# Performance work log

Measured on AMD Instinct MI355X. Metric: run time of the kernel, lower is better.

## Reference

```python
import jax, jax.numpy as jnp
import numpy as np

N_TABLES = 26
VOCAB = 100000
M_SPA = 64
B = 8192
N_DENSE = 13
N_FEAT = N_TABLES + 1  # 27 features entering interaction
LI, LJ = np.tril_indices(N_FEAT, k=-1)  # strictly-lower pairs, matches torch li/lj order


def setup_inputs() -> dict:
    key = jax.random.key(0)
    ks = jax.random.split(key, 16)
    dense_x = jax.random.normal(ks[0], (B, N_DENSE), dtype=jnp.float32)
    lS_i = jax.random.randint(ks[1], (N_TABLES, B), 0, VOCAB, dtype=jnp.int64)
    # one index per bag -> offsets are arange(B) for every table
    lS_o = jnp.tile(jnp.arange(B, dtype=jnp.int64)[None, :], (N_TABLES, 1))
    # embedding tables, uniform(-sqrt(1/n), sqrt(1/n)) as in create_emb
    s = np.sqrt(1.0 / VOCAB)
    Wemb = jax.random.uniform(ks[2], (N_TABLES, VOCAB, M_SPA), dtype=jnp.float32, minval=-s, maxval=s)

    def mk_lin(k, n, m):
        k1, k2 = jax.random.split(k)
        W = jax.random.normal(k1, (m, n), dtype=jnp.float32) * np.sqrt(2.0 / (m + n))
        b = jax.random.normal(k2, (m,), dtype=jnp.float32) * np.sqrt(1.0 / m)
        return W, b

    bW0, bb0 = mk_lin(ks[3], 13, 512)
    bW1, bb1 = mk_lin(ks[4], 512, 256)
    bW2, bb2 = mk_lin(ks[5], 256, 64)
    tW0, tb0 = mk_lin(ks[6], 415, 512)
    tW1, tb1 = mk_lin(ks[7], 512, 256)
    tW2, tb2 = mk_lin(ks[8], 256, 1)
    return dict(dense_x=dense_x, lS_i=lS_i, lS_o=lS_o, Wemb=Wemb,
                bW0=bW0, bb0=bb0, bW1=bW1, bb1=bb1, bW2=bW2, bb2=bb2,
                tW0=tW0, tb0=tb0, tW1=tW1, tb1=tb1, tW2=tW2, tb2=tb2)


def reference(dense_x, lS_i, lS_o, Wemb,
              bW0, bb0, bW1, bb1, bW2, bb2,
              tW0, tb0, tW1, tb1, tW2, tb2):
    # bottom MLP (all ReLU, sigmoid_bot=-1)
    x = jax.nn.relu(dense_x @ bW0.T + bb0)
    x = jax.nn.relu(x @ bW1.T + bb1)
    x = jax.nn.relu(x @ bW2.T + bb2)  # [B, 64]
    # multi-table EmbeddingBag(sum) with one index per bag == plain gather
    ly = jax.vmap(lambda W, idx: W[idx])(Wemb, lS_i)  # [26, B, 64]
    # dot interaction
    T = jnp.concatenate([x[:, None, :], jnp.transpose(ly, (1, 0, 2))], axis=1)  # [B, 27, 64]
    Z = jnp.einsum('bnd,bmd->bnm', T, T)  # [B, 27, 27]
    Zflat = Z[:, LI, LJ]  # [B, 351]
    R = jnp.concatenate([x, Zflat], axis=1)  # [B, 415]
    # top MLP: ReLU, ReLU, Sigmoid (sigmoid_top=2)
    z = jax.nn.relu(R @ tW0.T + tb0)
    z = jax.nn.relu(z @ tW1.T + tb1)
    p = jax.nn.sigmoid(z @ tW2.T + tb2)  # [B, 1]
    # loss_threshold = 0.0 -> no clamp
    return p
```

## Files before the change

### kernel.cpp

```cpp
#include <hip/hip_runtime.h>
#include <hip/hip_bf16.h>


typedef _Float16 f16x8 __attribute__((ext_vector_type(8)));
typedef float f32x4 __attribute__((ext_vector_type(4)));

__device__ __forceinline__ f16x8 cvt8(float4 a, float4 b) {
  f16x8 f;
  f[0] = (_Float16)a.x; f[1] = (_Float16)a.y;
  f[2] = (_Float16)a.z; f[3] = (_Float16)a.w;
  f[4] = (_Float16)b.x; f[5] = (_Float16)b.y;
  f[6] = (_Float16)b.z; f[7] = (_Float16)b.w;
  return f;
}

__device__ __forceinline__ void frag_store(
    _Float16* __restrict__ dst, const float* __restrict__ src,
    int fl, int Ksrc, int NKK)
{
  int lane = fl & 63, q = fl >> 6;
  int kk = q % NKK, j = q / NKK;
  int c = j * 16 + (lane & 15);
  int kb = kk * 32 + (lane >> 4) * 8;
  const float* s = src + (size_t)c * Ksrc + kb;
  f16x8 o;
#pragma unroll
  for (int e = 0; e < 8; ++e)
    o[e] = (_Float16)((kb + e < Ksrc) ? s[e] : 0.0f);
  *(f16x8*)&dst[(size_t)fl * 8] = o;
}

__global__ __launch_bounds__(256) void prep_kernel(
    const float* __restrict__ bW0, const float* __restrict__ bW1,
    const float* __restrict__ bW2, const float* __restrict__ tW0,
    const float* __restrict__ tW1,
    _Float16* __restrict__ w0, _Float16* __restrict__ w1,
    _Float16* __restrict__ w2, _Float16* __restrict__ t0,
    _Float16* __restrict__ t1)
{
  int f = blockIdx.x * 256 + threadIdx.x;
  if (f < 2048)  { frag_store(w0, bW0, f, 13, 1);  return; }
  f -= 2048;
  if (f < 16384) { frag_store(w1, bW1, f, 512, 16); return; }
  f -= 16384;
  if (f < 2048)  { frag_store(w2, bW2, f, 256, 8);  return; }
  f -= 2048;
  if (f < 28672) { frag_store(t0, tW0, f, 415, 14); return; }
  f -= 28672;
  if (f < 16384) { frag_store(t1, tW1, f, 512, 16); return; }
}

__global__ __launch_bounds__(1024, 1) void fused_kernel(
    const float* __restrict__ dense, const int* __restrict__ lSi,
    const float* __restrict__ Wemb,
    const _Float16* __restrict__ w0, const float* __restrict__ bb0,
    const _Float16* __restrict__ w1, const float* __restrict__ bb1,
    const _Float16* __restrict__ w2, const float* __restrict__ bb2,
    const _Float16* __restrict__ t0w, const float* __restrict__ tb0,
    const _Float16* __restrict__ t1w, const float* __restrict__ tb1,
    const float* __restrict__ tW2, const float* __restrict__ tb2,
    float* __restrict__ out)
{
  __shared__ __align__(16) char regA[32768];
  __shared__ __align__(16) char regB[28672];
  _Float16* x1s = (_Float16*)regA;
  _Float16* x3s = (_Float16*)regA;
  _Float16* z1s = (_Float16*)regA;
  float*    dns = (float*)regB;
  _Float16* x2s = (_Float16*)regB;
  _Float16* Rs  = (_Float16*)regB;
  float*    psm = (float*)regB;

  const int t = threadIdx.x;
  const int lane = t & 63, wv = t >> 6;
  const int rc = lane & 15, g = lane >> 4;
  const int ko = g * 8;
  const int sw = (rc & 7) << 3;
  const int b0 = blockIdx.x * 32;

  if (t < 416) {
    int r = t / 13, c = t - r * 13;
    dns[r * 16 + c] = dense[(size_t)b0 * 13 + t];
  } else if (t < 512) {
    int q = t - 416;
    int r = q / 3, c = 13 + (q - r * 3);
    dns[r * 16 + c] = 0.0f;
  }
  __syncthreads();

  {
    f16x8 af[2];
#pragma unroll
    for (int rt = 0; rt < 2; ++rt) {
      f16x8 a = {};
      if (g < 2) {
        const float* s = &dns[(rt * 16 + rc) * 16 + ko];
        a = cvt8(*(const float4*)s, *(const float4*)(s + 4));
      }
      af[rt] = a;
    }
    f32x4 acc[2][2] = {};
#pragma unroll
    for (int j = 0; j < 2; ++j) {
      const int jb = wv * 2 + j;
      f16x8 wf = *(const f16x8*)&w0[(size_t)(jb * 64 + lane) * 8];
#pragma unroll
      for (int rt = 0; rt < 2; ++rt)
        acc[rt][j] = __builtin_amdgcn_mfma_f32_16x16x32_f16(af[rt], wf, acc[rt][j], 0, 0, 0);
    }
#pragma unroll
    for (int j = 0; j < 2; ++j) {
      const int col = wv * 32 + j * 16 + rc;
      const float bs = bb0[col];
#pragma unroll
      for (int rt = 0; rt < 2; ++rt)
#pragma unroll
        for (int r = 0; r < 4; ++r) {
          int row = rt * 16 + g * 4 + r;
          float v = fmaxf(acc[rt][j][r] + bs, 0.0f);
          x1s[row * 512 + (col ^ ((row & 7) << 3))] = (_Float16)v;
        }
    }
  }
  __syncthreads();

  {
    f32x4 acc[2] = {};
#pragma unroll
    for (int kk = 0; kk < 16; ++kk) {
      f16x8 af[2];
#pragma unroll
      for (int rt = 0; rt < 2; ++rt)
        af[rt] = *(const f16x8*)&x1s[(rt * 16 + rc) * 512 + ((kk * 32 + ko) ^ sw)];
      f16x8 wf = *(const f16x8*)&w1[(size_t)((wv * 16 + kk) * 64 + lane) * 8];
#pragma unroll
      for (int rt = 0; rt < 2; ++rt)
        acc[rt] = __builtin_amdgcn_mfma_f32_16x16x32_f16(af[rt], wf, acc[rt], 0, 0, 0);
    }
    const int col = wv * 16 + rc;
    const float bs = bb1[col];
#pragma unroll
    for (int rt = 0; rt < 2; ++rt)
#pragma unroll
      for (int r = 0; r < 4; ++r) {
        int row = rt * 16 + g * 4 + r;
        float v = fmaxf(acc[rt][r] + bs, 0.0f);
        x2s[row * 256 + (col ^ ((row & 7) << 3))] = (_Float16)v;
      }
  }
  __syncthreads();

  if (wv < 8) {
    const int rt = wv & 1;
    const int cb = (wv >> 1) * 16;
    f32x4 acc = {};
#pragma unroll
    for (int kk = 0; kk < 8; ++kk) {
      f16x8 af = *(const f16x8*)&x2s[(rt * 16 + rc) * 256 + ((kk * 32 + ko) ^ sw)];
      f16x8 wf = *(const f16x8*)&w2[(size_t)(((cb >> 4) * 8 + kk) * 64 + lane) * 8];
      acc = __builtin_amdgcn_mfma_f32_16x16x32_f16(af, wf, acc, 0, 0, 0);
    }
    const int col = cb + rc;
    const float bs = bb2[col];
#pragma unroll
    for (int r = 0; r < 4; ++r) {
      int row = rt * 16 + g * 4 + r;
      float v = fmaxf(acc[r] + bs, 0.0f);
      x3s[row * 64 + col] = (_Float16)v;
    }
  }
  __syncthreads();

  {
    int e_idx[2][2];
#pragma unroll
    for (int i = 0; i < 2; ++i) {
      const int b = b0 + wv * 2 + i;
#pragma unroll
      for (int rt = 0; rt < 2; ++rt) {
        const int gr = rt * 16 + rc;
        e_idx[i][rt] = (gr >= 1 && gr <= 26) ? lSi[(size_t)(gr - 1) * 8192 + b] : 0;
      }
    }
#pragma unroll
    for (int i = 0; i < 2; ++i) {
      const int bl = wv * 2 + i;
      const int swr = (bl & 7) << 3;
      f16x8 frag[2][2];
#pragma unroll
      for (int rt = 0; rt < 2; ++rt) {
        const int gr = rt * 16 + rc;
        if (gr == 0) {
          frag[rt][0] = *(const f16x8*)&x3s[bl * 64 + ko];
          frag[rt][1] = *(const f16x8*)&x3s[bl * 64 + 32 + ko];
        } else if (gr <= 26) {
          const float* src = Wemb + ((size_t)(gr - 1) * 100000 + (size_t)e_idx[i][rt]) * 64;
#pragma unroll
          for (int kh = 0; kh < 2; ++kh) {
            const float* s = src + kh * 32 + ko;
            frag[rt][kh] = cvt8(*(const float4*)s, *(const float4*)(s + 4));
          }
        } else {
          f16x8 z = {};
          frag[rt][0] = z; frag[rt][1] = z;
        }
      }
      f32x4 z00 = {}, z10 = {}, z11 = {};
#pragma unroll
      for (int kh = 0; kh < 2; ++kh) {
        z00 = __builtin_amdgcn_mfma_f32_16x16x32_f16(frag[0][kh], frag[0][kh], z00, 0, 0, 0);
        z10 = __builtin_amdgcn_mfma_f32_16x16x32_f16(frag[1][kh], frag[0][kh], z10, 0, 0, 0);
        z11 = __builtin_amdgcn_mfma_f32_16x16x32_f16(frag[1][kh], frag[1][kh], z11, 0, 0, 0);
      }
      Rs[bl * 448 + (lane ^ swr)] = x3s[bl * 64 + lane];
      if (lane < 33) Rs[bl * 448 + ((415 + lane) ^ swr)] = (_Float16)0.0f;
      const int col = lane & 15;
      const int rr0 = (lane >> 4) * 4;
#pragma unroll
      for (int r = 0; r < 4; ++r) {
        const int i0 = rr0 + r;
        if (i0 > col) {
          int p = 64 + i0 * (i0 - 1) / 2 + col;
          Rs[bl * 448 + (p ^ swr)] = (_Float16)z00[r];
        }
        const int i1 = 16 + rr0 + r;
        if (i1 < 27) {
          int p = 64 + i1 * (i1 - 1) / 2 + col;
          Rs[bl * 448 + (p ^ swr)] = (_Float16)z10[r];
          const int j1 = 16 + col;
          if (i1 > j1) {
            int q = 64 + i1 * (i1 - 1) / 2 + j1;
            Rs[bl * 448 + (q ^ swr)] = (_Float16)z11[r];
          }
        }
      }
    }
  }
  __syncthreads();

  {
    f32x4 acc[2][2] = {};
#pragma unroll
    for (int kk = 0; kk < 14; ++kk) {
      f16x8 af[2];
#pragma unroll
      for (int rt = 0; rt < 2; ++rt)
        af[rt] = *(const f16x8*)&Rs[(rt * 16 + rc) * 448 + ((kk * 32 + ko) ^ sw)];
#pragma unroll
      for (int j = 0; j < 2; ++j) {
        const int jb = wv * 2 + j;
        f16x8 wf = *(const f16x8*)&t0w[(size_t)((jb * 14 + kk) * 64 + lane) * 8];
#pragma unroll
        for (int rt = 0; rt < 2; ++rt)
          acc[rt][j] = __builtin_amdgcn_mfma_f32_16x16x32_f16(af[rt], wf, acc[rt][j], 0, 0, 0);
      }
    }
#pragma unroll
    for (int j = 0; j < 2; ++j) {
      const int col = wv * 32 + j * 16 + rc;
      const float bs = tb0[col];
#pragma unroll
      for (int rt = 0; rt < 2; ++rt)
#pragma unroll
        for (int r = 0; r < 4; ++r) {
          int row = rt * 16 + g * 4 + r;
          float v = fmaxf(acc[rt][j][r] + bs, 0.0f);
          z1s[row * 512 + (col ^ ((row & 7) << 3))] = (_Float16)v;
        }
    }
  }
  __syncthreads();

  {
    f32x4 acc[2] = {};
#pragma unroll
    for (int kk = 0; kk < 16; ++kk) {
      f16x8 af[2];
#pragma unroll
      for (int rt = 0; rt < 2; ++rt)
        af[rt] = *(const f16x8*)&z1s[(rt * 16 + rc) * 512 + ((kk * 32 + ko) ^ sw)];
      f16x8 wf = *(const f16x8*)&t1w[(size_t)((wv * 16 + kk) * 64 + lane) * 8];
#pragma unroll
      for (int rt = 0; rt < 2; ++rt)
        acc[rt] = __builtin_amdgcn_mfma_f32_16x16x32_f16(af[rt], wf, acc[rt], 0, 0, 0);
    }
    const int col = wv * 16 + rc;
    const float bz = tb1[col];
    const float wz = tW2[col];
    float pd[2][4];
#pragma unroll
    for (int rt = 0; rt < 2; ++rt)
#pragma unroll
      for (int r = 0; r < 4; ++r)
        pd[rt][r] = fmaxf(acc[rt][r] + bz, 0.0f) * wz;
    __syncthreads();
#pragma unroll
    for (int rt = 0; rt < 2; ++rt)
#pragma unroll
      for (int r = 0; r < 4; ++r) {
        float v = pd[rt][r];
        v += __shfl_xor(v, 1, 64);
        v += __shfl_xor(v, 2, 64);
        v += __shfl_xor(v, 4, 64);
        v += __shfl_xor(v, 8, 64);
        if (rc == 0) psm[wv * 32 + rt * 16 + g * 4 + r] = v;
      }
  }
  __syncthreads();
  if (t < 32) {
    float s = tb2[0];
#pragma unroll
    for (int w = 0; w < 16; ++w) s += psm[w * 32 + t];
    out[b0 + t] = 1.0f / (1.0f + expf(-s));
  }
}

extern "C" void kernel_launch(void* const* d_in, const int* in_sizes, int n_in,
                              void* d_out, int out_size, void* d_ws, size_t ws_size,
                              hipStream_t stream)
{
  (void)in_sizes; (void)n_in; (void)out_size; (void)ws_size;
  const float* dense = (const float*)d_in[0];
  const int*   lSi   = (const int*)d_in[1];
  const float* Wemb  = (const float*)d_in[3];
  const float* bW0 = (const float*)d_in[4];  const float* bb0 = (const float*)d_in[5];
  const float* bW1 = (const float*)d_in[6];  const float* bb1 = (const float*)d_in[7];
  const float* bW2 = (const float*)d_in[8];  const float* bb2 = (const float*)d_in[9];
  const float* tW0 = (const float*)d_in[10]; const float* tb0 = (const float*)d_in[11];
  const float* tW1 = (const float*)d_in[12]; const float* tb1 = (const float*)d_in[13];
  const float* tW2 = (const float*)d_in[14]; const float* tb2 = (const float*)d_in[15];
  float* out = (float*)d_out;

  char* ws = (char*)d_ws;
  size_t off = 0;
  auto alloc = [&](size_t bytes) -> void* {
    void* p = ws + off;
    off += (bytes + 255) & ~(size_t)255;
    return p;
  };
  _Float16* w0 = (_Float16*)alloc((size_t)16384 * 2);
  _Float16* w1 = (_Float16*)alloc((size_t)131072 * 2);
  _Float16* w2 = (_Float16*)alloc((size_t)16384 * 2);
  _Float16* t0 = (_Float16*)alloc((size_t)229376 * 2);
  _Float16* t1 = (_Float16*)alloc((size_t)131072 * 2);

  prep_kernel<<<256, 256, 0, stream>>>(bW0, bW1, bW2, tW0, tW1,
                                       w0, w1, w2, t0, t1);
  fused_kernel<<<256, 1024, 0, stream>>>(dense, lSi, Wemb,
                                         w0, bb0, w1, bb1, w2, bb2,
                                         t0, tb0, t1, tb1, tW2, tb2, out);
}
```

Before: 36.66 us.

## Warp-specialize: prefetch half the embedding rows into LDS during bottom MLP

The bottom MLP now runs on only 8 of the 16 waves, each computing more output tiles. The other 8 waves issue asynchronous global-to-LDS loads (global_load_lds) for the first 12 tables' embedding rows while the MLP runs, and match its barriers with raw s_barrier calls. The interaction stage then reads those rows from swizzled LDS instead of global memory, so gather latency overlaps with MLP compute. In exchange it adds about 96KB of LDS and halves the MLP parallelism, and the barrier counts in the two branches must stay in lockstep.

Measured after the change: 36.70 us. Within noise of the previous version (+0.1%).

```diff
diff --git a/kernel.cpp b/kernel.cpp
--- a/kernel.cpp
+++ b/kernel.cpp
@@ -63,6 +63,7 @@
 {
   __shared__ __align__(16) char regA[32768];
   __shared__ __align__(16) char regB[28672];
+  __shared__ __align__(16) float embf[12 * 32 * 64];
   _Float16* x1s = (_Float16*)regA;
   _Float16* x3s = (_Float16*)regA;
   _Float16* z1s = (_Float16*)regA;
@@ -78,98 +79,142 @@
   const int sw = (rc & 7) << 3;
   const int b0 = blockIdx.x * 32;
 
-  if (t < 416) {
-    int r = t / 13, c = t - r * 13;
-    dns[r * 16 + c] = dense[(size_t)b0 * 13 + t];
-  } else if (t < 512) {
-    int q = t - 416;
-    int r = q / 3, c = 13 + (q - r * 3);
-    dns[r * 16 + c] = 0.0f;
-  }
-  __syncthreads();
-
-  {
-    f16x8 af[2];
-#pragma unroll
-    for (int rt = 0; rt < 2; ++rt) {
-      f16x8 a = {};
-      if (g < 2) {
-        const float* s = &dns[(rt * 16 + rc) * 16 + ko];
-        a = cvt8(*(const float4*)s, *(const float4*)(s + 4));
-      }
-      af[rt] = a;
-    }
-    f32x4 acc[2][2] = {};
-#pragma unroll
-    for (int j = 0; j < 2; ++j) {
-      const int jb = wv * 2 + j;
-      f16x8 wf = *(const f16x8*)&w0[(size_t)(jb * 64 + lane) * 8];
-#pragma unroll
-      for (int rt = 0; rt < 2; ++rt)
-        acc[rt][j] = __builtin_amdgcn_mfma_f32_16x16x32_f16(af[rt], wf, acc[rt][j], 0, 0, 0);
-    }
-#pragma unroll
-    for (int j = 0; j < 2; ++j) {
-      const int col = wv * 32 + j * 16 + rc;
-      const float bs = bb0[col];
+  if (wv < 8) {
+    if (t < 416) {
+      int r = t / 13, c = t - r * 13;
+      dns[r * 16 + c] = dense[(size_t)b0 * 13 + t];
+    } else if (t < 512) {
+      int q = t - 416;
+      int r = q / 3, c = 13 + (q - r * 3);
+      dns[r * 16 + c] = 0.0f;
+    }
+    __syncthreads();
+
+    {
+      f16x8 af[2];
+#pragma unroll
+      for (int rt = 0; rt < 2; ++rt) {
+        f16x8 a = {};
+        if (g < 2) {
+          const float* s = &dns[(rt * 16 + rc) * 16 + ko];
+          a = cvt8(*(const float4*)s, *(const float4*)(s + 4));
+        }
+        af[rt] = a;
+      }
+      f32x4 acc[2][4] = {};
+#pragma unroll
+      for (int j = 0; j < 4; ++j) {
+        const int jb = wv * 4 + j;
+        f16x8 wf = *(const f16x8*)&w0[(size_t)(jb * 64 + lane) * 8];
+#pragma unroll
+        for (int rt = 0; rt < 2; ++rt)
+          acc[rt][j] = __builtin_amdgcn_mfma_f32_16x16x32_f16(af[rt], wf, acc[rt][j], 0, 0, 0);
+      }
+#pragma unroll
+      for (int j = 0; j < 4; ++j) {
+        const int col = wv * 64 + j * 16 + rc;
+        const float bs = bb0[col];
+#pragma unroll
+        for (int rt = 0; rt < 2; ++rt)
+#pragma unroll
+          for (int r = 0; r < 4; ++r) {
+            int row = rt * 16 + g * 4 + r;
+            float v = fmaxf(acc[rt][j][r] + bs, 0.0f);
+            x1s[row * 512 + (col ^ ((row & 7) << 3))] = (_Float16)v;
+          }
+      }
+    }
+    __syncthreads();
+
+    {
+      f32x4 acc[2][2] = {};
+#pragma unroll
+      for (int kk = 0; kk < 16; ++kk) {
+        f16x8 af[2];
+#pragma unroll
+        for (int rt = 0; rt < 2; ++rt)
+          af[rt] = *(const f16x8*)&x1s[(rt * 16 + rc) * 512 + ((kk * 32 + ko) ^ sw)];
+#pragma unroll
+        for (int j = 0; j < 2; ++j) {
+          const int jb = wv * 2 + j;
+          f16x8 wf = *(const f16x8*)&w1[(size_t)((jb * 16 + kk) * 64 + lane) * 8];
+#pragma unroll
+          for (int rt = 0; rt < 2; ++rt)
+            acc[rt][j] = __builtin_amdgcn_mfma_f32_16x16x32_f16(af[rt], wf, acc[rt][j], 0, 0, 0);
+        }
+      }
+#pragma unroll
+      for (int j = 0; j < 2; ++j) {
+        const int col = wv * 32 + j * 16 + rc;
+        const float bs = bb1[col];
+#pragma unroll
+        for (int rt = 0; rt < 2; ++rt)
+#pragma unroll
+          for (int r = 0; r < 4; ++r) {
+            int row = rt * 16 + g * 4 + r;
+            float v = fmaxf(acc[rt][j][r] + bs, 0.0f);
+            x2s[row * 256 + (col ^ ((row & 7) << 3))] = (_Float16)v;
+          }
+      }
+    }
+    __syncthreads();
+
+    if (wv < 4) {
+      f32x4 acc[2] = {};
+#pragma unroll
+      for (int kk = 0; kk < 8; ++kk) {
+        f16x8 wf = *(const f16x8*)&w2[(size_t)((wv * 8 + kk) * 64 + lane) * 8];
+#pragma unroll
+        for (int rt = 0; rt < 2; ++rt) {
+          f16x8 af = *(const f16x8*)&x2s[(rt * 16 + rc) * 256 + ((kk * 32 + ko) ^ sw)];
+          acc[rt] = __builtin_amdgcn_mfma_f32_16x16x32_f16(af, wf, acc[rt], 0, 0, 0);
+        }
+      }
+      const int col = wv * 16 + rc;
+      const float bs = bb2[col];
 #pragma unroll
       for (int rt = 0; rt < 2; ++rt)
 #pragma unroll
         for (int r = 0; r < 4; ++r) {
           int row = rt * 16 + g * 4 + r;
-          float v = fmaxf(acc[rt][j][r] + bs, 0.0f);
-          x1s[row * 512 + (col ^ ((row & 7) << 3))] = (_Float16)v;
-        }
-    }
+          float v = fmaxf(acc[rt][r] + bs, 0.0f);
+          x3s[row * 64 + col] = (_Float16)v;
+        }
+    }
+    __syncthreads();
+  } else {
+    __builtin_amdgcn_s_barrier();
+    {
+      const int gw = wv - 8;
+      const int lhi = lane >> 4;
+      const int llo = lane & 15;
+      int idxv[12];
+#pragma unroll
+      for (int m = 0; m < 12; ++m) {
+        int q = gw * 12 + m;
+        int row = q * 4 + lhi;
+        int tb = row >> 5;
+        int bl = row & 31;
+        idxv[m] = lSi[(size_t)tb * 8192 + b0 + bl];
+      }
+#pragma unroll
+      for (int m = 0; m < 12; ++m) {
+        int q = gw * 12 + m;
+        int row = q * 4 + lhi;
+        int tb = row >> 5;
+        int cg = llo ^ (tb & 15);
+        const float* gp = Wemb + ((size_t)tb * 100000 + (size_t)idxv[m]) * 64 + cg * 4;
+        float* lp = &embf[q * 256];
+        __builtin_amdgcn_global_load_lds(
+            (const __attribute__((address_space(1))) void*)gp,
+            (__attribute__((address_space(3))) void*)lp, 16, 0, 0);
+      }
+    }
+    __builtin_amdgcn_s_barrier();
+    __builtin_amdgcn_s_barrier();
+    asm volatile("s_waitcnt vmcnt(0)" ::: "memory");
+    __builtin_amdgcn_s_barrier();
   }
-  __syncthreads();
-
-  {
-    f32x4 acc[2] = {};
-#pragma unroll
-    for (int kk = 0; kk < 16; ++kk) {
-      f16x8 af[2];
-#pragma unroll
-      for (int rt = 0; rt < 2; ++rt)
-        af[rt] = *(const f16x8*)&x1s[(rt * 16 + rc) * 512 + ((kk * 32 + ko) ^ sw)];
-      f16x8 wf = *(const f16x8*)&w1[(size_t)((wv * 16 + kk) * 64 + lane) * 8];
-#pragma unroll
-      for (int rt = 0; rt < 2; ++rt)
-        acc[rt] = __builtin_amdgcn_mfma_f32_16x16x32_f16(af[rt], wf, acc[rt], 0, 0, 0);
-    }
-    const int col = wv * 16 + rc;
-    const float bs = bb1[col];
-#pragma unroll
-    for (int rt = 0; rt < 2; ++rt)
-#pragma unroll
-      for (int r = 0; r < 4; ++r) {
-        int row = rt * 16 + g * 4 + r;
-        float v = fmaxf(acc[rt][r] + bs, 0.0f);
-        x2s[row * 256 + (col ^ ((row & 7) << 3))] = (_Float16)v;
-      }
-  }
-  __syncthreads();
-
-  if (wv < 8) {
-    const int rt = wv & 1;
-    const int cb = (wv >> 1) * 16;
-    f32x4 acc = {};
-#pragma unroll
-    for (int kk = 0; kk < 8; ++kk) {
-      f16x8 af = *(const f16x8*)&x2s[(rt * 16 + rc) * 256 + ((kk * 32 + ko) ^ sw)];
-      f16x8 wf = *(const f16x8*)&w2[(size_t)(((cb >> 4) * 8 + kk) * 64 + lane) * 8];
-      acc = __builtin_amdgcn_mfma_f32_16x16x32_f16(af, wf, acc, 0, 0, 0);
-    }
-    const int col = cb + rc;
-    const float bs = bb2[col];
-#pragma unroll
-    for (int r = 0; r < 4; ++r) {
-      int row = rt * 16 + g * 4 + r;
-      float v = fmaxf(acc[r] + bs, 0.0f);
-      x3s[row * 64 + col] = (_Float16)v;
-    }
-  }
-  __syncthreads();
 
   {
     int e_idx[2][2];
@@ -179,7 +224,7 @@
 #pragma unroll
       for (int rt = 0; rt < 2; ++rt) {
         const int gr = rt * 16 + rc;
-        e_idx[i][rt] = (gr >= 1 && gr <= 26) ? lSi[(size_t)(gr - 1) * 8192 + b] : 0;
+        e_idx[i][rt] = (gr >= 13 && gr <= 26) ? lSi[(size_t)(gr - 1) * 8192 + b] : 0;
       }
     }
 #pragma unroll
@@ -193,6 +238,17 @@
         if (gr == 0) {
           frag[rt][0] = *(const f16x8*)&x3s[bl * 64 + ko];
           frag[rt][1] = *(const f16x8*)&x3s[bl * 64 + 32 + ko];
+        } else if (gr <= 12) {
+          const int tb = gr - 1;
+          const float* eb = &embf[(tb * 32 + bl) * 64];
+#pragma unroll
+          for (int kh = 0; kh < 2; ++kh) {
+            int c0 = (kh * 8 + g * 2) ^ (tb & 15);
+            int c1 = (kh * 8 + g * 2 + 1) ^ (tb & 15);
+            float4 a = *(const float4*)(eb + c0 * 4);
+            float4 b4 = *(const float4*)(eb + c1 * 4);
+            frag[rt][kh] = cvt8(a, b4);
+          }
         } else if (gr <= 26) {
           const float* src = Wemb + ((size_t)(gr - 1) * 100000 + (size_t)e_idx[i][rt]) * 64;
 #pragma unroll
```
